# Kernel optimization log

Hardware: AMD Instinct MI355X
Metric: run time of the kernel (lower is better)

## Reference

```python
import jax, jax.numpy as jnp
import numpy as np
from jax import lax

ROI = 7          # roi_size
STRIDE = 16      # stride_prod
MH = MW = 24     # max crop height/width (fixed-size dynamic_slice window)


def setup_inputs() -> dict:
    key = jax.random.key(0)
    ks = jax.random.split(key, 12)
    N, C, Hf, Wf = 128, 512, 38, 38
    x = jax.random.normal(ks[0], (N, C, Hf, Wf), dtype=jnp.float32)
    # region_projs rows are (r, c, w, h): crop is x[:, c:c+h, r:r+w]
    r = jax.random.randint(ks[1], (N,), 0, 15)
    c = jax.random.randint(ks[2], (N,), 0, 15)
    w = jax.random.randint(ks[3], (N,), 4, MW + 1)
    h = jax.random.randint(ks[4], (N,), 4, MH + 1)
    region_projs = jnp.stack([r, c, w, h], axis=1).astype(jnp.int32)
    W1 = jax.random.normal(ks[5], (ROI * ROI * C, 4096), dtype=jnp.float32) * 0.01
    b1 = jnp.zeros((4096,), dtype=jnp.float32)
    W2 = jax.random.normal(ks[6], (4096, 4096), dtype=jnp.float32) * 0.01
    b2 = jnp.zeros((4096,), dtype=jnp.float32)
    Wcls = jax.random.normal(ks[7], (4096, 21), dtype=jnp.float32) * 0.01
    Wbox = jax.random.normal(ks[8], (4096, 80), dtype=jnp.float32) * 0.001
    return {"x": x, "region_projs": region_projs, "W1": W1, "b1": b1,
            "W2": W2, "b2": b2, "Wcls": Wcls, "Wbox": Wbox}


def _roi_adaptive_maxpool(crops, w, h):
    """crops: [N,C,MH,MW]; w,h: [N] int (valid extent). AdaptiveMaxPool2d((7,7)) per ROI."""
    ii = jnp.arange(ROI)
    ys = jnp.arange(MH)
    xs = jnp.arange(MW)
    # adaptive pool bin i of length L covers [floor(i*L/7), ceil((i+1)*L/7))
    rstart = (ii[None, :] * h[:, None]) // ROI            # [N,7]
    rend = ((ii[None, :] + 1) * h[:, None] + ROI - 1) // ROI
    cstart = (ii[None, :] * w[:, None]) // ROI
    cend = ((ii[None, :] + 1) * w[:, None] + ROI - 1) // ROI
    rmask = (ys[None, None, :] >= rstart[:, :, None]) & (ys[None, None, :] < rend[:, :, None])  # [N,7,MH]
    cmask = (xs[None, None, :] >= cstart[:, :, None]) & (xs[None, None, :] < cend[:, :, None])  # [N,7,MW]
    neg = jnp.float32(-jnp.inf)
    rows = [jnp.max(jnp.where(rmask[:, i, None, :, None], crops, neg), axis=2) for i in range(ROI)]
    tmp = jnp.stack(rows, axis=2)  # [N,C,7,MW]
    cols = [jnp.max(jnp.where(cmask[:, j, None, None, :], tmp, neg), axis=3) for j in range(ROI)]
    return jnp.stack(cols, axis=3)  # [N,C,7,7]


def reference(x, region_projs, W1, b1, W2, b2, Wcls, Wbox):
    N, C = x.shape[0], x.shape[1]
    # per-ROI crop: x[idx, :, c:c+h, r:r+w]; fixed-size window, bins mask the valid extent
    crops = jax.vmap(
        lambda xi, b: lax.dynamic_slice(xi, (0, b[1], b[0]), (C, MH, MW))
    )(x, region_projs)  # [N,C,MH,MW]
    pooled = _roi_adaptive_maxpool(crops, region_projs[:, 2], region_projs[:, 3])
    flat = pooled.reshape(N, -1)  # [N, 25088]
    # classifier (Dropout in eval mode = identity)
    h1 = jax.nn.relu(flat @ W1 + b1)
    h2 = jax.nn.relu(h1 @ W2 + b2)
    clf_scores = jax.nn.softmax(h2 @ Wcls, axis=1)          # [N,21]
    bbox_targets = h2 @ Wbox                                 # [N,80]
    # bbox_target_to_pred_bbox, vectorized over rois and classes
    bf = region_projs.astype(jnp.float32)
    r, c, w, h = bf[:, 0:1], bf[:, 1:2], bf[:, 2:3], bf[:, 3:4]  # [N,1]
    t = bbox_targets.reshape(N, 20, 4)
    p0 = jnp.ceil((w * t[..., 0] + r) * STRIDE) - 1.0
    p1 = jnp.ceil((h * t[..., 1] + c) * STRIDE) - 1.0
    p2 = jnp.floor(w * jnp.exp(t[..., 2]) * STRIDE) + 1.0
    p3 = jnp.floor(h * jnp.exp(t[..., 3]) * STRIDE) + 1.0
    bbox_pred = jnp.stack([p0, p1, p2, p3], axis=-1).reshape(N, 80)
    bbox_pred = lax.stop_gradient(bbox_pred)  # torch path detaches via math.ceil/floor
    return clf_scores, bbox_pred
```

## Files before the change

### kernel.cpp

```cpp
#include <hip/hip_runtime.h>
#include <hip/hip_bf16.h>
#include <math.h>

#define N_BATCH 128
#define C_CH    512
#define HF      38
#define WF      38
#define K1      25088
#define NH      4096
#define NCLS    21
#define NBOX    80
#define STEPS1  784
#define STEPS2  128

typedef __attribute__((ext_vector_type(8))) short s16x8;
typedef __attribute__((ext_vector_type(4))) float f32x4;

__device__ __forceinline__ unsigned short bf_rne(float x) {
  unsigned u = __float_as_uint(x);
  return (unsigned short)((u + 0x7FFFu + ((u >> 16) & 1u)) >> 16);
}

__device__ __forceinline__ void gload16(const void* g, void* l) {
  __builtin_amdgcn_global_load_lds(
      (const __attribute__((address_space(1))) unsigned int*)g,
      (__attribute__((address_space(3))) unsigned int*)l, 16, 0, 0);
}

__global__ __launch_bounds__(256) void pool_kernel(
    const float* __restrict__ x, const int* __restrict__ rp,
    unsigned short* __restrict__ Asw) {
  const int n = blockIdx.y, cb = blockIdx.x, tid = threadIdx.x;
  const int r = rp[n*4+0], c = rp[n*4+1], w = rp[n*4+2], h = rp[n*4+3];
  __shared__ float tile[8][24][25];
  __shared__ float pout[392];
  const int ch = tid >> 5, l32 = tid & 31;
  const float* xc = x + (((size_t)(n*C_CH + cb*8 + ch))*HF + c)*WF + r;
  for (int y = 0; y < h; ++y)
    for (int xx = l32; xx < w; xx += 32)
      tile[ch][y][xx] = xc[y*WF + xx];
  __syncthreads();
  for (int o = tid; o < 8*49; o += 256) {
    int ch2 = o / 49, ij = o - ch2*49, i = ij / 7, j = ij - i*7;
    int rs = (i*h)/7, re = ((i+1)*h + 6)/7;
    int cs = (j*w)/7, ce = ((j+1)*w + 6)/7;
    float m = -INFINITY;
    for (int y = rs; y < re; ++y)
      for (int xx = cs; xx < ce; ++xx)
        m = fmaxf(m, tile[ch2][y][xx]);
    pout[o] = m;
  }
  __syncthreads();
  if (tid < 49) {
    const int mt = n >> 4, mlo = n & 15;
    const int kl0 = tid * 8;
    const int kg0 = cb*392 + kl0;
    const int S = kg0 >> 5, kg = (kg0 >> 3) & 3;
    size_t base = ((size_t)S*8 + mt)*512 + (size_t)(kg*16 + mlo)*8;
    unsigned short q[8];
    #pragma unroll
    for (int e = 0; e < 8; ++e) q[e] = bf_rne(pout[kl0 + e]);
    ushort4 lo; lo.x=q[0]; lo.y=q[1]; lo.z=q[2]; lo.w=q[3];
    ushort4 hi; hi.x=q[4]; hi.y=q[5]; hi.z=q[6]; hi.w=q[7];
    *(ushort4*)(Asw + base)     = lo;
    *(ushort4*)(Asw + base + 4) = hi;
  }
}

template<int NT, int MINW>
__global__ __launch_bounds__(256, MINW) void gemm_v13(
    const unsigned short* __restrict__ Asw, const float* __restrict__ B,
    float* __restrict__ part, const int nsteps) {
  constexpr int NCOLS = NT * 16;
  constexpr int SB = 2 * NT;
  constexpr int LPR = NT * 4;
  constexpr int RPO = 64 / LPR;
  __shared__ float Bsm[4][2][32][NCOLS];
  const int tid = threadIdx.x, lane = tid & 63, wv = tid >> 6;
  const int wr = wv >> 1, wc = wv & 1;
  const int nb = blockIdx.x, ks = blockIdx.y;
  const int l15 = lane & 15, lq = lane >> 4;
  const unsigned short* Ag = Asw + (size_t)ks*nsteps*4096 + lane*8;
  const int srow = lane / LPR, scol = lane % LPR;
  const float* Bg = B + ((size_t)ks*nsteps*32 + srow)*NH
                  + (size_t)nb*(2*NCOLS) + wc*NCOLS;
  float* ldsb = &Bsm[wv][0][0][0];

  f32x4 acc[4][NT];
  #pragma unroll
  for (int i = 0; i < 4; ++i)
    #pragma unroll
    for (int j = 0; j < NT; ++j) acc[i][j] = (f32x4){0.f, 0.f, 0.f, 0.f};

  s16x8 w0[4];
#define LOADA(slot, g) do { \
    w0[slot] = *(const s16x8*)(Ag + (size_t)(g)*512); } while (0)

#define STAGEB(s, buf) do { \
    float* dst_ = ldsb + (buf)*(32*NCOLS); \
    _Pragma("unroll") \
    for (int i_ = 0; i_ < SB; ++i_) { \
      const int row_ = i_*RPO + srow; \
      gload16(Bg + ((size_t)(s)*32 + (size_t)i_*RPO)*NH \
                 + ((scol*4) ^ (8*((row_ >> 3) & 3))), dst_ + i_*256); \
    } } while (0)

  STAGEB(0, 0);
  LOADA(0, wr*4 + 0); LOADA(1, wr*4 + 1);
  LOADA(2, wr*4 + 2); LOADA(3, wr*4 + 3);

  for (int s = 0; s < nsteps; ++s) {
    if (s + 1 < nsteps) {
      STAGEB(s + 1, (s + 1) & 1);
      if constexpr (NT == 4) {
        asm volatile("s_waitcnt vmcnt(8)" ::: "memory");
      } else {
        asm volatile("s_waitcnt vmcnt(4)" ::: "memory");
      }
    } else {
      asm volatile("s_waitcnt vmcnt(0)" ::: "memory");
    }
    const float* bb = ldsb + (s & 1)*(32*NCOLS);
    s16x8 bf0[NT];
    #pragma unroll
    for (int nt = 0; nt < NT; ++nt) {
      #pragma unroll
      for (int e = 0; e < 8; ++e) {
        float xv = bb[(lq*8 + e)*NCOLS + ((nt*16 + l15) ^ (lq*8))];
        bf0[nt][e] = (short)bf_rne(xv);
      }
    }
    #pragma unroll
    for (int ml = 0; ml < 4; ++ml) {
      const s16x8 a0 = w0[ml];
      LOADA(ml, (s + 1)*8 + wr*4 + ml);
      #pragma unroll
      for (int nt = 0; nt < NT; ++nt)
        acc[ml][nt] = __builtin_amdgcn_mfma_f32_16x16x32_bf16(
            a0, bf0[nt], acc[ml][nt], 0, 0, 0);
    }
  }
#undef LOADA
#undef STAGEB
  float* Pb = part + (size_t)ks*N_BATCH*NH + (size_t)nb*(2*NCOLS) + wc*NCOLS;
  #pragma unroll
  for (int ml = 0; ml < 4; ++ml)
    #pragma unroll
    for (int nt = 0; nt < NT; ++nt)
      #pragma unroll
      for (int rr = 0; rr < 4; ++rr)
        Pb[(size_t)((wr*4 + ml)*16 + lq*4 + rr)*NH + nt*16 + l15]
            = acc[ml][nt][rr];
}

__global__ __launch_bounds__(256) void reduce_k(
    const float* __restrict__ part, const float* __restrict__ bias,
    unsigned short* __restrict__ AswOut, float* __restrict__ f32out,
    int KS, int mode) {
  const int idx = blockIdx.x*256 + threadIdx.x;
  float4 s = ((const float4*)part)[idx];
  for (int k2 = 1; k2 < KS; ++k2) {
    float4 p = ((const float4*)part)[(size_t)k2*131072 + idx];
    s.x += p.x; s.y += p.y; s.z += p.z; s.w += p.w;
  }
  float4 bv = ((const float4*)bias)[idx & 1023];
  float v[4];
  v[0] = fmaxf(s.x + bv.x, 0.f); v[1] = fmaxf(s.y + bv.y, 0.f);
  v[2] = fmaxf(s.z + bv.z, 0.f); v[3] = fmaxf(s.w + bv.w, 0.f);
  if (mode == 1) {
    float4 o; o.x = v[0]; o.y = v[1]; o.z = v[2]; o.w = v[3];
    ((float4*)f32out)[idx] = o;
  } else {
    int m = idx >> 10, k = (idx & 1023) * 4;
    int S = k >> 5, kg = (k >> 3) & 3, e0 = k & 7;
    size_t base = ((size_t)S*8 + (m >> 4))*512
                + (size_t)(kg*16 + (m & 15))*8 + e0;
    ushort4 st;
    st.x = bf_rne(v[0]); st.y = bf_rne(v[1]);
    st.z = bf_rne(v[2]); st.w = bf_rne(v[3]);
    *(ushort4*)(AswOut + base) = st;
  }
}

__global__ __launch_bounds__(256) void head_transpose(
    const float* __restrict__ Wcls, const float* __restrict__ Wbox,
    float* __restrict__ WT) {
  const int c = blockIdx.x;
  const float* src; int stride;
  if (c < NCLS) { src = Wcls + c; stride = NCLS; }
  else          { src = Wbox + (c - NCLS); stride = NBOX; }
  for (int k = threadIdx.x; k < NH; k += 256)
    WT[(size_t)c*NH + k] = src[(size_t)k*stride];
}

__global__ __launch_bounds__(512) void head_fused(
    const float* __restrict__ h2, const float* __restrict__ WT,
    const int* __restrict__ rp, float* __restrict__ out) {
  const int n = blockIdx.x, tid = threadIdx.x;
  const int wv = tid >> 6, lane = tid & 63;
  __shared__ float h2s[NH];
  __shared__ float dots[104];
  __shared__ float red[2];
  for (int i = tid; i < NH/4; i += 512)
    ((float4*)h2s)[i] = ((const float4*)(h2 + (size_t)n*NH))[i];
  __syncthreads();
  for (int c = wv; c < NCLS + NBOX; c += 8) {
    const float4* hp = (const float4*)h2s;
    const float4* wp = (const float4*)(WT + (size_t)c*NH);
    float s0=0.f, s1=0.f, s2=0.f, s3=0.f;
    #pragma unroll
    for (int it = 0; it < 16; ++it) {
      float4 a = hp[it*64 + lane];
      float4 b = wp[it*64 + lane];
      s0 = fmaf(a.x, b.x, s0); s1 = fmaf(a.y, b.y, s1);
      s2 = fmaf(a.z, b.z, s2); s3 = fmaf(a.w, b.w, s3);
    }
    float v = (s0 + s1) + (s2 + s3);
    #pragma unroll
    for (int m = 32; m >= 1; m >>= 1) v += __shfl_xor(v, m, 64);
    if (lane == 0) dots[c] = v;
  }
  __syncthreads();
  if (tid == 0) {
    float m = dots[0];
    for (int i = 1; i < NCLS; ++i) m = fmaxf(m, dots[i]);
    float s = 0.f;
    for (int i = 0; i < NCLS; ++i) s += expf(dots[i] - m);
    red[0] = m; red[1] = s;
  }
  __syncthreads();
  if (tid < NCLS) {
    out[(size_t)n*NCLS + tid] = expf(dots[tid] - red[0]) / red[1];
  } else if (tid < NCLS + NBOX) {
    const int j = tid - NCLS;
    const float t  = dots[tid];
    const float rf = (float)rp[n*4+0];
    const float cf = (float)rp[n*4+1];
    const float wf = (float)rp[n*4+2];
    const float hf = (float)rp[n*4+3];
    float p;
    switch (j & 3) {
      case 0:  p = ceilf (__fmul_rn(__fadd_rn(__fmul_rn(wf, t), rf), 16.f)) - 1.f; break;
      case 1:  p = ceilf (__fmul_rn(__fadd_rn(__fmul_rn(hf, t), cf), 16.f)) - 1.f; break;
      case 2:  p = floorf(__fmul_rn(__fmul_rn(wf, expf(t)), 16.f)) + 1.f; break;
      default: p = floorf(__fmul_rn(__fmul_rn(hf, expf(t)), 16.f)) + 1.f; break;
    }
    out[(size_t)N_BATCH*NCLS + (size_t)n*NBOX + j] = p;
  }
}

extern "C" void kernel_launch(void* const* d_in, const int* in_sizes, int n_in,
                              void* d_out, int out_size, void* d_ws, size_t ws_size,
                              hipStream_t stream) {
  const float* x    = (const float*)d_in[0];
  const int*   rp   = (const int*)  d_in[1];
  const float* W1   = (const float*)d_in[2];
  const float* b1   = (const float*)d_in[3];
  const float* W2   = (const float*)d_in[4];
  const float* b2   = (const float*)d_in[5];
  const float* Wcls = (const float*)d_in[6];
  const float* Wbox = (const float*)d_in[7];
  float* out = (float*)d_out;

  char* wp = (char*)d_ws;
  unsigned short* Asw1 = (unsigned short*)wp; wp += (size_t)STEPS1*8192;
  unsigned short* Asw2 = (unsigned short*)wp; wp += (size_t)STEPS2*8192;
  float* h2f = (float*)wp;            wp += (size_t)N_BATCH*NH*4;
  float* WT  = (float*)wp;            wp += (size_t)(NCLS+NBOX)*NH*4;
  float* part = (float*)wp;
  const size_t fixed = (size_t)(wp - (char*)d_ws);
  const size_t slab = (size_t)N_BATCH*NH*4;
  int KS1 = 16, KS2 = 8;
  if (fixed + 16*slab > ws_size) { KS1 = 8; KS2 = 8; }

  pool_kernel<<<dim3(64, 128), 256, 0, stream>>>(x, rp, Asw1);
  head_transpose<<<dim3(NCLS + NBOX), 256, 0, stream>>>(Wcls, Wbox, WT);

  gemm_v13<4, 2><<<dim3(32, KS1), 256, 0, stream>>>(Asw1, W1, part, STEPS1/KS1);
  reduce_k<<<dim3(512), 256, 0, stream>>>(part, b1, Asw2, nullptr, KS1, 0);

  gemm_v13<2, 3><<<dim3(64, KS2), 256, 0, stream>>>(Asw2, W2, part, STEPS2/KS2);
  reduce_k<<<dim3(512), 256, 0, stream>>>(part, b2, nullptr, h2f, KS2, 1);

  head_fused<<<dim3(128), 512, 0, stream>>>(h2f, WT, rp, out);
}
```

Measured before the change: 251.3 us.

## Stage A and B tiles through shared LDS with block-wide double buffering

Replaces the per-wave private B staging and direct global A register loads with a block-cooperative scheme. All four waves load both the A tile (8 KB) and a 128-column B tile (16 KB) into double-buffered shared memory, synchronised by __syncthreads. This lets a B tile be shared across both wave rows instead of each wave fetching its own, cutting redundant global traffic. The second GEMM now uses the same NT=4 config with a split-K of 16 instead of 8. In exchange it adds block-level barriers every step and larger LDS use, which may limit occupancy and overlap.

Result: faster. 244.9 us (-2.6%).

```diff
diff --git a/kernel.cpp b/kernel.cpp
--- a/kernel.cpp
+++ b/kernel.cpp
@@ -67,86 +67,75 @@
   }
 }
 
-template<int NT, int MINW>
-__global__ __launch_bounds__(256, MINW) void gemm_v13(
+__global__ __launch_bounds__(256, 3) void gemm_v14(
     const unsigned short* __restrict__ Asw, const float* __restrict__ B,
     float* __restrict__ part, const int nsteps) {
-  constexpr int NCOLS = NT * 16;
-  constexpr int SB = 2 * NT;
-  constexpr int LPR = NT * 4;
-  constexpr int RPO = 64 / LPR;
-  __shared__ float Bsm[4][2][32][NCOLS];
+  __shared__ char smem[49152];
   const int tid = threadIdx.x, lane = tid & 63, wv = tid >> 6;
   const int wr = wv >> 1, wc = wv & 1;
   const int nb = blockIdx.x, ks = blockIdx.y;
   const int l15 = lane & 15, lq = lane >> 4;
-  const unsigned short* Ag = Asw + (size_t)ks*nsteps*4096 + lane*8;
-  const int srow = lane / LPR, scol = lane % LPR;
-  const float* Bg = B + ((size_t)ks*nsteps*32 + srow)*NH
-                  + (size_t)nb*(2*NCOLS) + wc*NCOLS;
-  float* ldsb = &Bsm[wv][0][0][0];
-
-  f32x4 acc[4][NT];
+  const float* Bg0 = B + (size_t)nb * 128;
+
+  f32x4 acc[4][4];
   #pragma unroll
   for (int i = 0; i < 4; ++i)
     #pragma unroll
-    for (int j = 0; j < NT; ++j) acc[i][j] = (f32x4){0.f, 0.f, 0.f, 0.f};
-
-  s16x8 w0[4];
-#define LOADA(slot, g) do { \
-    w0[slot] = *(const s16x8*)(Ag + (size_t)(g)*512); } while (0)
-
-#define STAGEB(s, buf) do { \
-    float* dst_ = ldsb + (buf)*(32*NCOLS); \
+    for (int j = 0; j < 4; ++j) acc[i][j] = (f32x4){0.f, 0.f, 0.f, 0.f};
+
+#define STAGE(s, bufb) do { \
+    char* Ad = smem + (bufb); \
+    char* Bd = smem + (bufb) + 8192; \
     _Pragma("unroll") \
-    for (int i_ = 0; i_ < SB; ++i_) { \
-      const int row_ = i_*RPO + srow; \
-      gload16(Bg + ((size_t)(s)*32 + (size_t)i_*RPO)*NH \
-                 + ((scol*4) ^ (8*((row_ >> 3) & 3))), dst_ + i_*256); \
+    for (int t_ = 0; t_ < 6; ++t_) { \
+      const int i_ = wv*6 + t_; \
+      if (i_ < 8) { \
+        gload16((const char*)Asw + (((size_t)(ks*nsteps + (s))*8 + i_) << 10) \
+                    + lane*16, \
+                Ad + (i_ << 10)); \
+      } else { \
+        const int j_ = i_ - 8; \
+        const int row_ = 2*j_ + (lane >> 5); \
+        const int gc_ = ((lane & 31)*4) ^ (8*((row_ >> 3) & 3)); \
+        gload16(Bg0 + ((size_t)(ks*nsteps + (s))*32 + row_)*NH + gc_, \
+                Bd + (j_ << 10)); \
+      } \
     } } while (0)
 
-  STAGEB(0, 0);
-  LOADA(0, wr*4 + 0); LOADA(1, wr*4 + 1);
-  LOADA(2, wr*4 + 2); LOADA(3, wr*4 + 3);
-
+  STAGE(0, 0);
+  __syncthreads();
+
+  int bufb = 0;
   for (int s = 0; s < nsteps; ++s) {
-    if (s + 1 < nsteps) {
-      STAGEB(s + 1, (s + 1) & 1);
-      if constexpr (NT == 4) {
-        asm volatile("s_waitcnt vmcnt(8)" ::: "memory");
-      } else {
-        asm volatile("s_waitcnt vmcnt(4)" ::: "memory");
-      }
-    } else {
-      asm volatile("s_waitcnt vmcnt(0)" ::: "memory");
-    }
-    const float* bb = ldsb + (s & 1)*(32*NCOLS);
-    s16x8 bf0[NT];
-    #pragma unroll
-    for (int nt = 0; nt < NT; ++nt) {
+    if (s + 1 < nsteps) STAGE(s + 1, bufb ^ 24576);
+    const char* Ab = smem + bufb;
+    const float* Bf = (const float*)(smem + bufb + 8192);
+    s16x8 bf0[4];
+    #pragma unroll
+    for (int nt = 0; nt < 4; ++nt) {
       #pragma unroll
       for (int e = 0; e < 8; ++e) {
-        float xv = bb[(lq*8 + e)*NCOLS + ((nt*16 + l15) ^ (lq*8))];
+        float xv = Bf[(lq*8 + e)*128 + ((wc*64 + nt*16 + l15) ^ (8*lq))];
         bf0[nt][e] = (short)bf_rne(xv);
       }
     }
     #pragma unroll
     for (int ml = 0; ml < 4; ++ml) {
-      const s16x8 a0 = w0[ml];
-      LOADA(ml, (s + 1)*8 + wr*4 + ml);
+      const s16x8 a0 = *(const s16x8*)(Ab + ((wr*4 + ml) << 10) + lane*16);
       #pragma unroll
-      for (int nt = 0; nt < NT; ++nt)
+      for (int nt = 0; nt < 4; ++nt)
         acc[ml][nt] = __builtin_amdgcn_mfma_f32_16x16x32_bf16(
             a0, bf0[nt], acc[ml][nt], 0, 0, 0);
     }
-  }
-#undef LOADA
-#undef STAGEB
-  float* Pb = part + (size_t)ks*N_BATCH*NH + (size_t)nb*(2*NCOLS) + wc*NCOLS;
+    __syncthreads();
+    bufb ^= 24576;
+  }
+#undef STAGE
+  float* Pb = part + (size_t)ks*N_BATCH*NH + (size_t)nb*128 + wc*64;
   #pragma unroll
   for (int ml = 0; ml < 4; ++ml)
     #pragma unroll
-    for (int nt = 0; nt < NT; ++nt)
+    for (int nt = 0; nt < 4; ++nt)
       #pragma unroll
       for (int rr = 0; rr < 4; ++rr)
         Pb[(size_t)((wr*4 + ml)*16 + lq*4 + rr)*NH + nt*16 + l15]
@@ -270,16 +259,16 @@
   float* part = (float*)wp;
   const size_t fixed = (size_t)(wp - (char*)d_ws);
   const size_t slab = (size_t)N_BATCH*NH*4;
-  int KS1 = 16, KS2 = 8;
+  int KS1 = 16, KS2 = 16;
   if (fixed + 16*slab > ws_size) { KS1 = 8; KS2 = 8; }
 
   pool_kernel<<<dim3(64, 128), 256, 0, stream>>>(x, rp, Asw1);
   head_transpose<<<dim3(NCLS + NBOX), 256, 0, stream>>>(Wcls, Wbox, WT);
 
-  gemm_v13<4, 2><<<dim3(32, KS1), 256, 0, stream>>>(Asw1, W1, part, STEPS1/KS1);
+  gemm_v14<<<dim3(32, KS1), 256, 0, stream>>>(Asw1, W1, part, STEPS1/KS1);
   reduce_k<<<dim3(512), 256, 0, stream>>>(part, b1, Asw2, nullptr, KS1, 0);
 
-  gemm_v13<2, 3><<<dim3(64, KS2), 256, 0, stream>>>(Asw2, W2, part, STEPS2/KS2);
+  gemm_v14<<<dim3(32, KS2), 256, 0, stream>>>(Asw2, W2, part, STEPS2/KS2);
   reduce_k<<<dim3(512), 256, 0, stream>>>(part, b2, nullptr, h2f, KS2, 1);
 
   head_fused<<<dim3(128), 512, 0, stream>>>(h2f, WT, rp, out);
```

## Triple-buffer B staging and use narrower tiles for first GEMM

Applied to the files above, without the earlier changes.

The GEMM kernel now stages B through a three-deep LDS ring buffer with two steps of prefetch in flight, where it used double buffering. It is also fixed to 32-column tiles per wave (NT=2), so GEMM1 launches twice as many column blocks (64 instead of 32). The deeper prefetch is meant to hide global-load latency on the weight stream, and the extra blocks give GEMM1 more parallelism. In exchange, A fragments are reloaded for more column blocks and each block uses more LDS.

Result: slower. 299.2 us (+19.0%).

```diff
diff --git a/kernel.cpp b/kernel.cpp
--- a/kernel.cpp
+++ b/kernel.cpp
@@ -67,66 +67,59 @@
   }
 }
 
-template<int NT, int MINW>
-__global__ __launch_bounds__(256, MINW) void gemm_v13(
+template<int MINW>
+__global__ __launch_bounds__(256, MINW) void gemm_v15(
     const unsigned short* __restrict__ Asw, const float* __restrict__ B,
     float* __restrict__ part, const int nsteps) {
-  constexpr int NCOLS = NT * 16;
-  constexpr int SB = 2 * NT;
-  constexpr int LPR = NT * 4;
-  constexpr int RPO = 64 / LPR;
-  __shared__ float Bsm[4][2][32][NCOLS];
+  __shared__ float Bsm[4][3][32][32];
   const int tid = threadIdx.x, lane = tid & 63, wv = tid >> 6;
   const int wr = wv >> 1, wc = wv & 1;
   const int nb = blockIdx.x, ks = blockIdx.y;
   const int l15 = lane & 15, lq = lane >> 4;
   const unsigned short* Ag = Asw + (size_t)ks*nsteps*4096 + lane*8;
-  const int srow = lane / LPR, scol = lane % LPR;
+  const int srow = lane >> 3, scol = lane & 7;
   const float* Bg = B + ((size_t)ks*nsteps*32 + srow)*NH
-                  + (size_t)nb*(2*NCOLS) + wc*NCOLS;
+                  + (size_t)nb*64 + wc*32;
   float* ldsb = &Bsm[wv][0][0][0];
 
-  f32x4 acc[4][NT];
+  f32x4 acc[4][2];
   #pragma unroll
   for (int i = 0; i < 4; ++i)
     #pragma unroll
-    for (int j = 0; j < NT; ++j) acc[i][j] = (f32x4){0.f, 0.f, 0.f, 0.f};
+    for (int j = 0; j < 2; ++j) acc[i][j] = (f32x4){0.f, 0.f, 0.f, 0.f};
 
   s16x8 w0[4];
 #define LOADA(slot, g) do { \
     w0[slot] = *(const s16x8*)(Ag + (size_t)(g)*512); } while (0)
 
 #define STAGEB(s, buf) do { \
-    float* dst_ = ldsb + (buf)*(32*NCOLS); \
+    float* dst_ = ldsb + (buf)*1024; \
     _Pragma("unroll") \
-    for (int i_ = 0; i_ < SB; ++i_) { \
-      const int row_ = i_*RPO + srow; \
-      gload16(Bg + ((size_t)(s)*32 + (size_t)i_*RPO)*NH \
+    for (int i_ = 0; i_ < 4; ++i_) { \
+      const int row_ = i_*8 + srow; \
+      gload16(Bg + ((size_t)(s)*32 + (size_t)i_*8)*NH \
                  + ((scol*4) ^ (8*((row_ >> 3) & 3))), dst_ + i_*256); \
     } } while (0)
 
-  STAGEB(0, 0);
+  STAGEB(0, 0); STAGEB(1, 1);
   LOADA(0, wr*4 + 0); LOADA(1, wr*4 + 1);
   LOADA(2, wr*4 + 2); LOADA(3, wr*4 + 3);
 
+  int b2 = 2;
   for (int s = 0; s < nsteps; ++s) {
-    if (s + 1 < nsteps) {
-      STAGEB(s + 1, (s + 1) & 1);
-      if constexpr (NT == 4) {
-        asm volatile("s_waitcnt vmcnt(8)" ::: "memory");
-      } else {
-        asm volatile("s_waitcnt vmcnt(4)" ::: "memory");
-      }
+    if (s + 2 < nsteps) {
+      STAGEB(s + 2, b2);
+      asm volatile("s_waitcnt vmcnt(12)" ::: "memory");
     } else {
       asm volatile("s_waitcnt vmcnt(0)" ::: "memory");
     }
-    const float* bb = ldsb + (s & 1)*(32*NCOLS);
-    s16x8 bf0[NT];
-    #pragma unroll
-    for (int nt = 0; nt < NT; ++nt) {
+    const float* bb = ldsb + (s % 3)*1024;
+    s16x8 bf0[2];
+    #pragma unroll
+    for (int nt = 0; nt < 2; ++nt) {
       #pragma unroll
       for (int e = 0; e < 8; ++e) {
-        float xv = bb[(lq*8 + e)*NCOLS + ((nt*16 + l15) ^ (lq*8))];
+        float xv = bb[(lq*8 + e)*32 + ((nt*16 + l15) ^ (8*lq))];
         bf0[nt][e] = (short)bf_rne(xv);
       }
     }
@@ -135,18 +128,19 @@
       const s16x8 a0 = w0[ml];
       LOADA(ml, (s + 1)*8 + wr*4 + ml);
       #pragma unroll
-      for (int nt = 0; nt < NT; ++nt)
+      for (int nt = 0; nt < 2; ++nt)
         acc[ml][nt] = __builtin_amdgcn_mfma_f32_16x16x32_bf16(
             a0, bf0[nt], acc[ml][nt], 0, 0, 0);
     }
+    b2 = (b2 == 2) ? 0 : b2 + 1;
   }
 #undef LOADA
 #undef STAGEB
-  float* Pb = part + (size_t)ks*N_BATCH*NH + (size_t)nb*(2*NCOLS) + wc*NCOLS;
+  float* Pb = part + (size_t)ks*N_BATCH*NH + (size_t)nb*64 + wc*32;
   #pragma unroll
   for (int ml = 0; ml < 4; ++ml)
     #pragma unroll
-    for (int nt = 0; nt < NT; ++nt)
+    for (int nt = 0; nt < 2; ++nt)
       #pragma unroll
       for (int rr = 0; rr < 4; ++rr)
         Pb[(size_t)((wr*4 + ml)*16 + lq*4 + rr)*NH + nt*16 + l15]
@@ -276,10 +270,10 @@
   pool_kernel<<<dim3(64, 128), 256, 0, stream>>>(x, rp, Asw1);
   head_transpose<<<dim3(NCLS + NBOX), 256, 0, stream>>>(Wcls, Wbox, WT);
 
-  gemm_v13<4, 2><<<dim3(32, KS1), 256, 0, stream>>>(Asw1, W1, part, STEPS1/KS1);
+  gemm_v15<3><<<dim3(64, KS1), 256, 0, stream>>>(Asw1, W1, part, STEPS1/KS1);
   reduce_k<<<dim3(512), 256, 0, stream>>>(part, b1, Asw2, nullptr, KS1, 0);
 
-  gemm_v13<2, 3><<<dim3(64, KS2), 256, 0, stream>>>(Asw2, W2, part, STEPS2/KS2);
+  gemm_v15<3><<<dim3(64, KS2), 256, 0, stream>>>(Asw2, W2, part, STEPS2/KS2);
   reduce_k<<<dim3(512), 256, 0, stream>>>(part, b2, nullptr, h2f, KS2, 1);
 
   head_fused<<<dim3(128), 512, 0, stream>>>(h2f, WT, rp, out);
```
